# Performance work log

Measured on AMD Instinct MI355X. Metric: run time of the kernel, lower is better.

Reference implementation:

```python
import jax, jax.numpy as jnp
import numpy as np

N_LEVELS = 8
F_DIM = 8
N_SIDE = 2 ** (N_LEVELS - 1)
N_PIX = 12 * N_SIDE * N_SIDE  # hp.nside2npix(128) = 196608
BATCH = 1_000_000


def setup_inputs() -> dict:
    key = jax.random.key(0)
    keys = jax.random.split(key, 2 + N_LEVELS)
    kp, kw, kidx = keys[0], keys[1], keys[2:]
    # nn.init.uniform_(params[i], a=-1e-4, b=1e-4)
    params = jax.random.uniform(kp, (N_LEVELS, N_PIX, F_DIM),
                                dtype=jnp.float32, minval=-1e-4, maxval=1e-4)
    # healpy neighbor pixels per level: valid range [0, 12*4**i) for nside=2**i
    neigh_pix = jnp.stack([
        jax.random.randint(kidx[i], (4, BATCH), 0, 12 * 4 ** i, dtype=jnp.int32)
        for i in range(N_LEVELS)
    ], axis=0)  # [L, 4, B]
    # bilinear interpolation weights sum to 1 over the 4 neighbors
    w = jax.random.uniform(kw, (N_LEVELS, 4, BATCH), dtype=jnp.float32) + 1e-3
    neigh_weight = w / jnp.sum(w, axis=1, keepdims=True)  # [L, 4, B]
    return {"params": params, "neigh_pix": neigh_pix, "neigh_weight": neigh_weight}


def reference(params, neigh_pix, neigh_weight):
    # params: [L, N_PIX, F]; neigh_pix, neigh_weight: [L, 4, B]
    lvl = jnp.arange(N_LEVELS)[:, None, None]        # [L,1,1]
    gathered = params[lvl, neigh_pix]                # [L, 4, B, F]
    # weighted sum over the 4 neighbors (torch: multiply then sum(dim=0) per level)
    reps = jnp.einsum('lnbf,lnb->lbf', gathered, neigh_weight)  # [L, B, F]
    # torch.stack(..., dim=-1) -> [B, F, L], then reshape(B, F*L)
    batch = neigh_pix.shape[-1]
    out = jnp.transpose(reps, (1, 2, 0)).reshape(batch, F_DIM * N_LEVELS)
    return out.astype(jnp.float32)
```

## Files before the change

kernel.cpp:

```cpp
#include <hip/hip_runtime.h>

#define N_LEVELS 8
#define F_DIM 8
#define N_PIX (12 * 128 * 128)
#define PACKED_ROWS 262140
#define PACKED_BYTES ((size_t)PACKED_ROWS * F_DIM * 2)

using f32x4 = __attribute__((ext_vector_type(4))) float;
using u16x8 = __attribute__((ext_vector_type(8))) unsigned short;

__device__ __forceinline__ unsigned short f32_to_bf16_rne(float x) {
    unsigned u = __float_as_uint(x);
    return (unsigned short)((u + 0x7fffu + ((u >> 16) & 1u)) >> 16);
}

__device__ __forceinline__ float bf16_hi_to_f32(unsigned short h) {
    return __uint_as_float(((unsigned)h) << 16);
}

__global__ __launch_bounds__(256) void pack_params_bf16(
    const float* __restrict__ params, unsigned short* __restrict__ packed)
{
    int l = blockIdx.y;
    unsigned rows = 12u << (2 * l);
    unsigned r = blockIdx.x * 256 + threadIdx.x;
    if (r >= rows) return;
    const f32x4* src = (const f32x4*)(params + ((size_t)l * N_PIX + r) * F_DIM);
    f32x4 a = __builtin_nontemporal_load(src);
    f32x4 c = __builtin_nontemporal_load(src + 1);
    unsigned rowoff = ((1u << (2 * l)) - 1u) * 4u;
    u16x8 o;
    o[0] = f32_to_bf16_rne(a[0]); o[1] = f32_to_bf16_rne(a[1]);
    o[2] = f32_to_bf16_rne(a[2]); o[3] = f32_to_bf16_rne(a[3]);
    o[4] = f32_to_bf16_rne(c[0]); o[5] = f32_to_bf16_rne(c[1]);
    o[6] = f32_to_bf16_rne(c[2]); o[7] = f32_to_bf16_rne(c[3]);
    *(u16x8*)(packed + ((size_t)(rowoff + r) << 3)) = o;
}

__global__ __launch_bounds__(256, 4) void heal_enc_bf16_v3(
    const unsigned short* __restrict__ packed,
    const int*   __restrict__ pix,
    const float* __restrict__ wgt,
    float*       __restrict__ out,
    int batch)
{
    __shared__ float stage[128][68];

    const int tl = threadIdx.x;
    const int t  = blockIdx.x * 256 + tl;
    const int b  = t >> 1;
    const int h  = t & 1;
    const int rl = tl >> 1;

    if (b < batch) {
        const size_t sb = (size_t)batch;

        float acc[32];
#pragma unroll
        for (int i = 0; i < 32; ++i) acc[i] = 0.f;

        int   idx[4][4];
        float w[4][4];
#pragma unroll
        for (int lr = 0; lr < 4; ++lr) {
            const int l = h * 4 + lr;
            const size_t base = (size_t)(l * 4) * sb + (size_t)b;
#pragma unroll
            for (int n = 0; n < 4; ++n) {
                idx[lr][n] = __builtin_nontemporal_load(pix + base + (size_t)n * sb);
                w[lr][n]   = __builtin_nontemporal_load(wgt + base + (size_t)n * sb);
            }
        }

#pragma unroll
        for (int c = 0; c < 2; ++c) {
            u16x8 row[2][4];
#pragma unroll
            for (int lr2 = 0; lr2 < 2; ++lr2) {
                const int lr = c * 2 + lr2;
                const int l  = h * 4 + lr;
                const unsigned ro = ((1u << (2 * l)) - 1u) * 4u;
#pragma unroll
                for (int n = 0; n < 4; ++n)
                    row[lr2][n] = *(const u16x8*)(
                        packed + ((size_t)(ro + (unsigned)idx[lr][n]) << 3));
            }
#pragma unroll
            for (int lr2 = 0; lr2 < 2; ++lr2) {
                const int lr = c * 2 + lr2;
#pragma unroll
                for (int n = 0; n < 4; ++n) {
#pragma unroll
                    for (int f = 0; f < 8; ++f)
                        acc[lr * 8 + f] =
                            fmaf(w[lr][n], bf16_hi_to_f32(row[lr2][n][f]),
                                 acc[lr * 8 + f]);
                }
            }
        }

#pragma unroll
        for (int f = 0; f < 8; ++f) {
#pragma unroll
            for (int lr = 0; lr < 4; ++lr)
                stage[rl][f * 8 + h * 4 + lr] = acc[lr * 8 + f];
        }
    }
    __syncthreads();

    const int blockRow0 = blockIdx.x * 128;
#pragma unroll
    for (int k = 0; k < 8; ++k) {
        const int idx16 = k * 256 + tl;
        const int row   = idx16 >> 4;
        const int chunk = idx16 & 15;
        const int bb    = blockRow0 + row;
        if (bb < batch) {
            f32x4 v = *(const f32x4*)&stage[row][chunk * 4];
            __builtin_nontemporal_store(
                v, (f32x4*)(out + (size_t)bb * (F_DIM * N_LEVELS)) + chunk);
        }
    }
}

__global__ __launch_bounds__(256) void heal_enc_f32(
    const float* __restrict__ params,
    const int*   __restrict__ pix,
    const float* __restrict__ wgt,
    float*       __restrict__ out,
    int batch)
{
    int b = blockIdx.x * 256 + threadIdx.x;
    if (b >= batch) return;
    const size_t sb = (size_t)batch;
    float acc[64];
#pragma unroll
    for (int l = 0; l < N_LEVELS; ++l) {
        float4 r0 = make_float4(0.f, 0.f, 0.f, 0.f);
        float4 r1 = make_float4(0.f, 0.f, 0.f, 0.f);
#pragma unroll
        for (int n = 0; n < 4; ++n) {
            size_t off = (size_t)(l * 4 + n) * sb + (size_t)b;
            int   idx = pix[off];
            float w   = wgt[off];
            const float4* row =
                (const float4*)(params + ((size_t)l * N_PIX + (size_t)idx) * F_DIM);
            float4 p0 = row[0];
            float4 p1 = row[1];
            r0.x = fmaf(w, p0.x, r0.x); r0.y = fmaf(w, p0.y, r0.y);
            r0.z = fmaf(w, p0.z, r0.z); r0.w = fmaf(w, p0.w, r0.w);
            r1.x = fmaf(w, p1.x, r1.x); r1.y = fmaf(w, p1.y, r1.y);
            r1.z = fmaf(w, p1.z, r1.z); r1.w = fmaf(w, p1.w, r1.w);
        }
        acc[0*8+l] = r0.x; acc[1*8+l] = r0.y; acc[2*8+l] = r0.z; acc[3*8+l] = r0.w;
        acc[4*8+l] = r1.x; acc[5*8+l] = r1.y; acc[6*8+l] = r1.z; acc[7*8+l] = r1.w;
    }
    float4* o = (float4*)(out + (size_t)b * (F_DIM * N_LEVELS));
#pragma unroll
    for (int c = 0; c < 16; ++c)
        o[c] = make_float4(acc[4*c+0], acc[4*c+1], acc[4*c+2], acc[4*c+3]);
}

extern "C" void kernel_launch(void* const* d_in, const int* in_sizes, int n_in,
                              void* d_out, int out_size, void* d_ws, size_t ws_size,
                              hipStream_t stream)
{
    const float* params = (const float*)d_in[0];
    const int*   pix    = (const int*)d_in[1];
    const float* wgt    = (const float*)d_in[2];
    float*       out    = (float*)d_out;

    int batch = in_sizes[2] / (N_LEVELS * 4);

    if (ws_size >= PACKED_BYTES) {
        unsigned short* packed = (unsigned short*)d_ws;
        dim3 pgrid((N_PIX + 255) / 256, N_LEVELS);
        pack_params_bf16<<<pgrid, 256, 0, stream>>>(params, packed);
        int grid = (2 * batch + 255) / 256;
        heal_enc_bf16_v3<<<grid, 256, 0, stream>>>(packed, pix, wgt, out, batch);
    } else {
        int grid = (batch + 255) / 256;
        heal_enc_f32<<<grid, 256, 0, stream>>>(params, pix, wgt, out, batch);
    }
}
```

Baseline: 501.1 us.

## Cache coarse-level bf16 table in LDS and split levels by half-block

Each block copies the packed bf16 rows for levels 0-3 (1020 rows, about 16KB) into shared memory. Threads in the first half of the block gather those coarse levels from LDS, and the second half gathers levels 4-7 from global memory. The thread mapping changes from interleaved pairs to half-block groups. The output staging now uses vector writes with an XOR swizzle to avoid bank conflicts. Every block pays for the 16KB table load, and occupancy drops to 3 blocks per SM. Work is also unbalanced: the global-gather half does the slow loads while the LDS half finishes early.

Result: faster. 485.8 us (-3.1%).

```diff
diff --git a/kernel.cpp b/kernel.cpp
--- a/kernel.cpp
+++ b/kernel.cpp
@@ -5,6 +5,7 @@
 #define N_PIX (12 * 128 * 128)
 #define PACKED_ROWS 262140
 #define PACKED_BYTES ((size_t)PACKED_ROWS * F_DIM * 2)
+#define SMALL_ROWS 1020
 
 using f32x4 = __attribute__((ext_vector_type(4))) float;
 using u16x8 = __attribute__((ext_vector_type(8))) unsigned short;
@@ -37,7 +38,7 @@
     *(u16x8*)(packed + ((size_t)(rowoff + r) << 3)) = o;
 }
 
-__global__ __launch_bounds__(256, 4) void heal_enc_bf16_v3(
+__global__ __launch_bounds__(256, 3) void heal_enc_bf16_v4(
     const unsigned short* __restrict__ packed,
     const int*   __restrict__ pix,
     const float* __restrict__ wgt,
@@ -45,19 +46,25 @@
     int batch)
 {
     __shared__ float stage[128][68];
+    __shared__ u16x8 table[SMALL_ROWS];
 
     const int tl = threadIdx.x;
-    const int t  = blockIdx.x * 256 + tl;
-    const int b  = t >> 1;
-    const int h  = t & 1;
-    const int rl = tl >> 1;
+
+#pragma unroll
+    for (int i = 0; i < 4; ++i) {
+        int r = i * 256 + tl;
+        if (r < SMALL_ROWS)
+            table[r] = *(const u16x8*)(packed + ((size_t)r << 3));
+    }
+
+    const int rl = tl & 127;
+    const int h  = tl >> 7;
+    const int b  = blockIdx.x * 128 + rl;
+
+    __syncthreads();
 
     if (b < batch) {
         const size_t sb = (size_t)batch;
-
-        float acc[32];
-#pragma unroll
-        for (int i = 0; i < 32; ++i) acc[i] = 0.f;
 
         int   idx[4][4];
         float w[4][4];
@@ -72,38 +79,61 @@
             }
         }
 
-#pragma unroll
-        for (int c = 0; c < 2; ++c) {
-            u16x8 row[2][4];
-#pragma unroll
-            for (int lr2 = 0; lr2 < 2; ++lr2) {
-                const int lr = c * 2 + lr2;
-                const int l  = h * 4 + lr;
-                const unsigned ro = ((1u << (2 * l)) - 1u) * 4u;
+        float acc[32];
+#pragma unroll
+        for (int i = 0; i < 32; ++i) acc[i] = 0.f;
+
+        if (h == 0) {
+            u16x8 row[4][4];
+#pragma unroll
+            for (int lr = 0; lr < 4; ++lr) {
+                const unsigned ro = ((1u << (2 * lr)) - 1u) * 4u;
 #pragma unroll
                 for (int n = 0; n < 4; ++n)
-                    row[lr2][n] = *(const u16x8*)(
-                        packed + ((size_t)(ro + (unsigned)idx[lr][n]) << 3));
+                    row[lr][n] = table[ro + (unsigned)idx[lr][n]];
             }
 #pragma unroll
-            for (int lr2 = 0; lr2 < 2; ++lr2) {
-                const int lr = c * 2 + lr2;
-#pragma unroll
-                for (int n = 0; n < 4; ++n) {
+            for (int lr = 0; lr < 4; ++lr)
+#pragma unroll
+                for (int n = 0; n < 4; ++n)
 #pragma unroll
                     for (int f = 0; f < 8; ++f)
-                        acc[lr * 8 + f] =
-                            fmaf(w[lr][n], bf16_hi_to_f32(row[lr2][n][f]),
-                                 acc[lr * 8 + f]);
+                        acc[lr * 8 + f] = fmaf(
+                            w[lr][n], bf16_hi_to_f32(row[lr][n][f]),
+                            acc[lr * 8 + f]);
+        } else {
+#pragma unroll
+            for (int c = 0; c < 2; ++c) {
+                u16x8 row[2][4];
+#pragma unroll
+                for (int lr2 = 0; lr2 < 2; ++lr2) {
+                    const int lr = c * 2 + lr2;
+                    const int l  = 4 + lr;
+                    const unsigned ro = ((1u << (2 * l)) - 1u) * 4u;
+#pragma unroll
+                    for (int n = 0; n < 4; ++n)
+                        row[lr2][n] = *(const u16x8*)(
+                            packed + ((size_t)(ro + (unsigned)idx[lr][n]) << 3));
+                }
+#pragma unroll
+                for (int lr2 = 0; lr2 < 2; ++lr2) {
+                    const int lr = c * 2 + lr2;
+#pragma unroll
+                    for (int n = 0; n < 4; ++n)
+#pragma unroll
+                        for (int f = 0; f < 8; ++f)
+                            acc[lr * 8 + f] = fmaf(
+                                w[lr][n], bf16_hi_to_f32(row[lr2][n][f]),
+                                acc[lr * 8 + f]);
                 }
             }
         }
 
 #pragma unroll
         for (int f = 0; f < 8; ++f) {
-#pragma unroll
-            for (int lr = 0; lr < 4; ++lr)
-                stage[rl][f * 8 + h * 4 + lr] = acc[lr * 8 + f];
+            f32x4 v = { acc[0 * 8 + f], acc[1 * 8 + f],
+                        acc[2 * 8 + f], acc[3 * 8 + f] };
+            *(f32x4*)&stage[rl][4 * ((2 * f + h) ^ (rl & 7))] = v;
         }
     }
     __syncthreads();
@@ -116,7 +146,7 @@
         const int chunk = idx16 & 15;
         const int bb    = blockRow0 + row;
         if (bb < batch) {
-            f32x4 v = *(const f32x4*)&stage[row][chunk * 4];
+            f32x4 v = *(const f32x4*)&stage[row][4 * (chunk ^ (row & 7))];
             __builtin_nontemporal_store(
                 v, (f32x4*)(out + (size_t)bb * (F_DIM * N_LEVELS)) + chunk);
         }
@@ -176,8 +206,8 @@
         unsigned short* packed = (unsigned short*)d_ws;
         dim3 pgrid((N_PIX + 255) / 256, N_LEVELS);
         pack_params_bf16<<<pgrid, 256, 0, stream>>>(params, packed);
-        int grid = (2 * batch + 255) / 256;
-        heal_enc_bf16_v3<<<grid, 256, 0, stream>>>(packed, pix, wgt, out, batch);
+        int grid = (batch + 127) / 128;
+        heal_enc_bf16_v4<<<grid, 256, 0, stream>>>(packed, pix, wgt, out, batch);
     } else {
         int grid = (batch + 255) / 256;
         heal_enc_f32<<<grid, 256, 0, stream>>>(params, pix, wgt, out, batch);
```
